# Optimization experiments

Measured on AMD Instinct MI355X. Metric: run time of the kernel, lower is better.

The kernel has to match this reference:

```python
import jax, jax.numpy as jnp
import numpy as np

N_QUBITS = 16
DEPTH = 4
BATCH = 512

# Convention: wire 0 is the most-significant bit of the state index (PennyLane default).

def _rx(t):
    # t: scalar or (B,) real angle -> (2,2) or (B,2,2) complex RX matrix
    h = 0.5 * t
    c = jnp.cos(h).astype(jnp.complex64)
    s = (-1j * jnp.sin(h)).astype(jnp.complex64)
    return jnp.stack([jnp.stack([c, s], -1), jnp.stack([s, c], -1)], -2)

def _ry(t):
    h = 0.5 * t
    c = jnp.cos(h).astype(jnp.complex64)
    s = jnp.sin(h).astype(jnp.complex64)
    return jnp.stack([jnp.stack([c, -s], -1), jnp.stack([s, c], -1)], -2)

def _rz(t):
    e = jnp.exp(-0.5j * t.astype(jnp.complex64))  # diag(e^{-it/2}, e^{+it/2})
    z = jnp.zeros_like(e)
    return jnp.stack([jnp.stack([e, z], -1), jnp.stack([z, jnp.conj(e)], -1)], -2)

def _apply_1q(state, U, q, n):
    # state: (B, 2^n); U: (2,2) shared or (B,2,2) per-batch
    B = state.shape[0]
    L, R = 2 ** q, 2 ** (n - q - 1)
    s = state.reshape(B, L, 2, R)
    if U.ndim == 2:
        s = jnp.einsum('ij,bljr->blir', U, s)
    else:
        s = jnp.einsum('bij,bljr->blir', U, s)
    return s.reshape(B, -1)

def _apply_cnot(state, c, t, n):
    # flips target bit t where control bit c == 1
    B = state.shape[0]
    a, b = min(c, t), max(c, t)
    s = state.reshape(B, 2 ** a, 2, 2 ** (b - a - 1), 2, 2 ** (n - b - 1))
    if c < t:
        # control axis=2, target axis=4
        s1 = s[:, :, 1]                      # (B, 2^a, mid, 2, rest)
        flipped = s1[:, :, :, ::-1, :]
        s = jnp.stack([s[:, :, 0], flipped], axis=2)
    else:
        # control axis=4, target axis=2
        s1 = s[:, :, :, :, 1, :]             # (B, 2^a, 2, mid, rest)
        flipped = s1[:, :, ::-1]
        s = jnp.stack([s[:, :, :, :, 0, :], flipped], axis=4)
    return s.reshape(B, -1)

def _circuit(x, params):
    B, n = x.shape
    depth = params.shape[0]
    state = jnp.zeros((B, 2 ** n), jnp.complex64).at[:, 0].set(1.0)
    # data encoding: batched RX per wire
    for i in range(n):
        state = _apply_1q(state, _rx(x[:, i]), i, n)
    for layer in range(depth):
        for i in range(n):
            # circuit applies RZ then RX then RY -> fuse into one 2x2 matrix
            U = _ry(params[layer, i, 2]) @ _rx(params[layer, i, 1]) @ _rz(params[layer, i, 0])
            state = _apply_1q(state, U, i, n)
        for i in range(n - 1):
            state = _apply_cnot(state, i, i + 1, n)
        state = _apply_cnot(state, n - 1, 0, n)
    # <Z_i> = P(bit_i = 0) - P(bit_i = 1)
    probs = state.real ** 2 + state.imag ** 2
    expz = []
    for i in range(n):
        p = probs.reshape(B, 2 ** i, 2, 2 ** (n - i - 1))
        expz.append(p[:, :, 0].sum((1, 2)) - p[:, :, 1].sum((1, 2)))
    return jnp.stack(expz, axis=1)  # (B, n_qubits)


def setup_inputs() -> dict:
    key = jax.random.key(0)
    k1, k2 = jax.random.split(key)
    x = jax.random.normal(k1, (BATCH, N_QUBITS), dtype=jnp.float32)
    params = jax.random.normal(k2, (DEPTH, N_QUBITS, 3), dtype=jnp.float32)
    return {"x": x, "params": params}


def reference(x, params):
    return _circuit(x, params)
```

## Files before the change

### kernel.cpp

```cpp
#include <hip/hip_runtime.h>


#define NQ 16
#define TPB 256

typedef float __attribute__((ext_vector_type(2))) f2;

__device__ __forceinline__ f2 f2s(float s) { return (f2){s, s}; }

__device__ __forceinline__ f2 cfma(f2 u, f2 a, f2 acc) {
    f2 as = { -a.y, a.x };
    acc = __builtin_elementwise_fma(f2s(u.x), a,  acc);
    acc = __builtin_elementwise_fma(f2s(u.y), as, acc);
    return acc;
}

__device__ __forceinline__ f2 cmulpk(f2 a, f2 b) {
    f2 bs = { -b.y, b.x };
    f2 r = f2s(a.x) * b;
    return __builtin_elementwise_fma(f2s(a.y), bs, r);
}

__device__ __forceinline__ void computeU(const float* params, int layer, int q, f2* U) {
    const float* p = params + (layer*NQ + q)*3;
    float s0, c0, s1, c1, s2, c2;
    sincosf(0.5f*p[0], &s0, &c0);
    sincosf(0.5f*p[1], &s1, &c1);
    sincosf(0.5f*p[2], &s2, &c2);
    f2 m00 = { c1*c0, -c1*s0};
    f2 m01 = { s1*s0, -s1*c0};
    f2 m10 = {-s1*s0, -s1*c0};
    f2 m11 = { c1*c0,  c1*s0};
    U[0] = c2*m00 - s2*m10;
    U[1] = c2*m01 - s2*m11;
    U[2] = s2*m00 + c2*m10;
    U[3] = s2*m01 + c2*m11;
}

template<int MASK>
__device__ __forceinline__ void gate32(f2* A, f2 u00, f2 u01, f2 u10, f2 u11) {
    #pragma unroll
    for (int a = 0; a < 32; ++a) {
        if (!(a & MASK)) {
            f2 x = A[a], y = A[a | MASK];
            f2 xs = { -x.y, x.x };
            f2 ys = { -y.y, y.x };
            f2 nx = f2s(u00.x) * x;
            nx = __builtin_elementwise_fma(f2s(u00.y), xs, nx);
            nx = __builtin_elementwise_fma(f2s(u01.x), y,  nx);
            nx = __builtin_elementwise_fma(f2s(u01.y), ys, nx);
            f2 ny = f2s(u10.x) * x;
            ny = __builtin_elementwise_fma(f2s(u10.y), xs, ny);
            ny = __builtin_elementwise_fma(f2s(u11.x), y,  ny);
            ny = __builtin_elementwise_fma(f2s(u11.y), ys, ny);
            A[a] = nx; A[a | MASK] = ny;
        }
    }
}

__device__ __forceinline__ constexpr int permB(int ad) {
    return (ad & 1)
         | ((((ad >> 1) ^ (ad >> 2)) & 1) << 1)
         | ((((ad >> 2) ^ (ad >> 3)) & 1) << 2)
         | ((((ad >> 3) ^ (ad >> 4)) & 1) << 3)
         | ((((ad >> 4) ^  ad      ) & 1) << 4);
}

__global__ __launch_bounds__(TPB) void qc_gen(
    const float* __restrict__ x, const float* __restrict__ params,
    f2* __restrict__ st)
{
    __shared__ f2 V[16][2];
    const int t    = threadIdx.x;
    const int b    = blockIdx.x >> 3;
    const int fix3 = blockIdx.x & 7;
    f2* base = st + ((size_t)b << NQ) + (fix3 << 13);

    if (t < 16) {
        f2 U[4];
        computeU(params, 0, t, U);
        float s, c;
        sincosf(0.5f * x[b*NQ + t], &s, &c);
        V[15 - t][0] = (f2){U[0].x*c + U[1].y*s, U[0].y*c - U[1].x*s};
        V[15 - t][1] = (f2){U[2].x*c + U[3].y*s, U[2].y*c - U[3].x*s};
    }
    __syncthreads();

    f2 cf = cmulpk(V[0][fix3 & 1], V[1][(fix3 >> 1) & 1]);
    cf = cmulpk(cf, V[2][(fix3 >> 2) & 1]);
    #pragma unroll
    for (int bb = 1; bb <= 7; ++bb)
        cf = cmulpk(cf, V[3 + bb][((t >> (bb - 1)) ^ (t >> bb)) & 1]);

    const int t0 = t & 1, t7 = (t >> 7) & 1;
    float4* dst = (float4*)base;
    #pragma unroll
    for (int h = 0; h < 2; ++h) {
        #pragma unroll
        for (int k = 0; k < 8; ++k) {
            const int k0 = k & 1, k1 = (k >> 1) & 1, k2 = (k >> 2) & 1;
            f2 pk = cmulpk(cf, V[11][t7 ^ k0]);
            pk = cmulpk(pk, V[12][k0 ^ k1]);
            pk = cmulpk(pk, V[13][k1 ^ k2]);
            pk = cmulpk(pk, V[14][k2 ^ h]);
            pk = cmulpk(pk, V[15][h]);
            f2 w0 = cmulpk(pk, V[3][t0]);
            f2 w1 = cmulpk(pk, V[3][1 ^ t0]);
            dst[(t + 256*k) | (h << 11)] = make_float4(w0.x, w0.y, w1.x, w1.y);
        }
    }
}

__global__ __launch_bounds__(TPB, 4) void qc_B_heavy(
    const float* __restrict__ params, f2* __restrict__ st, int lm)
{
    __shared__ __align__(16) f2 S[4096];
    __shared__ f2 Ush[13][4];

    const int t    = threadIdx.x;
    const int b    = blockIdx.x >> 3;
    const int fixb = blockIdx.x & 7;
    f2* base = st + ((size_t)b << NQ);

    if (t < 13) {
        int qb = (t == 0) ? 12 : (t == 1) ? 0 : (t < 5) ? (17 - t) : (16 - t);
        computeU(params, lm, qb, Ush[t]);
    }

    f2 R[32];
    #pragma unroll
    for (int k = 0; k < 16; ++k) {
        int j = 2*(t + 256*k);
        int m = (j & 511) | (fixb << 9) | (((j >> 9) & 1) << 12) | ((j >> 10) << 13);
        float4 v = *(const float4*)(base + m);
        R[2*k]   = (f2){v.x, v.y};
        R[2*k+1] = (f2){v.z, v.w};
    }
    f2 A[32];
    #pragma unroll
    for (int a = 0; a < 32; ++a) A[a] = R[permB(a)];
    __syncthreads();

    gate32<1> (A, Ush[0][0],  Ush[0][1],  Ush[0][2],  Ush[0][3]);
    gate32<2> (A, Ush[1][0],  Ush[1][1],  Ush[1][2],  Ush[1][3]);
    gate32<4> (A, Ush[2][0],  Ush[2][1],  Ush[2][2],  Ush[2][3]);
    gate32<8> (A, Ush[3][0],  Ush[3][1],  Ush[3][2],  Ush[3][3]);
    gate32<16>(A, Ush[4][0],  Ush[4][1],  Ush[4][2],  Ush[4][3]);

    #pragma unroll
    for (int h = 0; h < 2; ++h) {
        __syncthreads();
        #pragma unroll
        for (int c = 0; c < 8; ++c) {
            int slot = ((t << 1) | (c << 9)) ^ (((t >> 4) & 7) << 1);
            f2 a0 = A[h*16 + 2*c], a1 = A[h*16 + 2*c + 1];
            *(float4*)&S[slot] = make_float4(a0.x, a0.y, a1.x, a1.y);
        }
        __syncthreads();
        #pragma unroll
        for (int rr = 0; rr < 16; ++rr) {
            int jj = (t & 1) | (rr << 1) | (((t >> 1) & 15) << 5) | (((t >> 5) & 7) << 9);
            A[h*16 + rr] = S[jj ^ (((t >> 1) & 7) << 1)];
        }
    }

    gate32<1>(A, Ush[5][0], Ush[5][1], Ush[5][2], Ush[5][3]);
    gate32<2>(A, Ush[6][0], Ush[6][1], Ush[6][2], Ush[6][3]);
    gate32<4>(A, Ush[7][0], Ush[7][1], Ush[7][2], Ush[7][3]);
    gate32<8>(A, Ush[8][0], Ush[8][1], Ush[8][2], Ush[8][3]);

    #pragma unroll
    for (int h = 0; h < 2; ++h) {
        __syncthreads();
        #pragma unroll
        for (int rr = 0; rr < 16; ++rr) {
            int jj = (t & 1) | (rr << 1) | (((t >> 1) & 15) << 5) | (((t >> 5) & 7) << 9);
            S[jj ^ (((t >> 1) & 7) << 1)] = A[h*16 + rr];
        }
        __syncthreads();
        #pragma unroll
        for (int rr = 0; rr < 16; ++rr) {
            int jj = (t & 31) | (rr << 5) | (((t >> 5) & 7) << 9);
            A[h*16 + rr] = S[jj ^ ((rr & 7) << 1)];
        }
    }

    gate32<1>(A, Ush[9][0],  Ush[9][1],  Ush[9][2],  Ush[9][3]);
    gate32<2>(A, Ush[10][0], Ush[10][1], Ush[10][2], Ush[10][3]);
    gate32<4>(A, Ush[11][0], Ush[11][1], Ush[11][2], Ush[11][3]);
    gate32<8>(A, Ush[12][0], Ush[12][1], Ush[12][2], Ush[12][3]);

    #pragma unroll
    for (int h = 0; h < 2; ++h) {
        #pragma unroll
        for (int rr = 0; rr < 16; ++rr) {
            int d = (t & 31) | (rr << 5) | (((t >> 5) & 7) << 9) | (h << 12);
            int m = (d & 511) | (fixb << 9) | (((d >> 9) & 1) << 12) | ((d >> 10) << 13);
            base[m] = A[h*16 + rr];
        }
    }
}

__global__ __launch_bounds__(TPB, 4) void qc_A_lite(
    const float* __restrict__ params, f2* __restrict__ st, int layer)
{
    __shared__ __align__(16) f2 S[4096];
    __shared__ f2 Ush[3][4];
    const int t    = threadIdx.x;
    const int b    = blockIdx.x >> 3;
    const int fix3 = blockIdx.x & 7;
    f2* base = st + ((size_t)b << NQ) + (fix3 << 13);

    if (t < 3) computeU(params, layer, 3 - t, Ush[t]);

    f2 A[32];
    const float4* src = (const float4*)base;
    #pragma unroll
    for (int k = 0; k < 16; ++k) {
        float4 v = src[t + 256*k];
        A[2*k]   = (f2){v.x, v.y};
        A[2*k+1] = (f2){v.z, v.w};
    }
    __syncthreads();

    gate32<2>(A, Ush[0][0], Ush[0][1], Ush[0][2], Ush[0][3]);
    gate32<4>(A, Ush[1][0], Ush[1][1], Ush[1][2], Ush[1][3]);
    gate32<8>(A, Ush[2][0], Ush[2][1], Ush[2][2], Ush[2][3]);

    float4* dst = (float4*)base;
    #pragma unroll
    for (int h = 0; h < 2; ++h) {
        __syncthreads();
        #pragma unroll
        for (int c = 0; c < 8; ++c) {
            int slot = ((t << 1) | (c << 9)) ^ (((t >> 4) & 7) << 1);
            f2 a0 = A[h*16 + 2*c], a1 = A[h*16 + 2*c + 1];
            *(float4*)&S[slot] = make_float4(a0.x, a0.y, a1.x, a1.y);
        }
        __syncthreads();
        #pragma unroll
        for (int k = 0; k < 8; ++k) {
            int d  = 2*(t + 256*k);
            int i0 = d ^ (d >> 1) ^ (h << 11);
            int i1 = (d+1) ^ ((d+1) >> 1) ^ (h << 11);
            f2 a0 = S[i0 ^ (((i0 >> 5) & 7) << 1)];
            f2 a1 = S[i1 ^ (((i1 >> 5) & 7) << 1)];
            dst[(t + 256*k) | (h << 11)] = make_float4(a0.x, a0.y, a1.x, a1.y);
        }
    }
}

__global__ __launch_bounds__(TPB) void qc_A_final(
    const float* __restrict__ params, const f2* __restrict__ st,
    float* __restrict__ out)
{
    __shared__ f2 Ush[3][4];
    const int t    = threadIdx.x;
    const int b    = blockIdx.x >> 3;
    const int fix3 = blockIdx.x & 7;
    const f2* base = st + ((size_t)b << NQ) + (fix3 << 13);

    if (t < 3) computeU(params, 3, 3 - t, Ush[t]);

    f2 A[32];
    const float4* src = (const float4*)base;
    #pragma unroll
    for (int k = 0; k < 16; ++k) {
        float4 v = src[t + 256*k];
        A[2*k]   = (f2){v.x, v.y};
        A[2*k+1] = (f2){v.z, v.w};
    }
    __syncthreads();

    gate32<2>(A, Ush[0][0], Ush[0][1], Ush[0][2], Ush[0][3]);
    gate32<4>(A, Ush[1][0], Ush[1][1], Ush[1][2], Ush[1][3]);
    gate32<8>(A, Ush[2][0], Ush[2][1], Ush[2][2], Ush[2][3]);

    float m1 = 0.f, m2 = 0.f, m3 = 0.f, m4 = 0.f, m5 = 0.f;
    #pragma unroll
    for (int a = 0; a < 32; ++a) {
        float p = A[a].x*A[a].x + A[a].y*A[a].y;
        m1 += (__popc(a & 0x1E) & 1) ? -p : p;
        m2 += (__popc(a & 0x1F) & 1) ? -p : p;
        m3 += (__popc(a & 0x1C) & 1) ? -p : p;
        m4 += (__popc(a & 0x18) & 1) ? -p : p;
        m5 += (__popc(a & 0x0F) & 1) ? -p : p;
    }
    const int pt = __popc(t) & 1;
    const int pf = __popc(fix3) & 1;
    float acc[NQ];
    acc[0] = ((pt ^ pf) & 1) ? -m5 : m5;
    acc[1] = m4;
    acc[2] = m3;
    acc[3] = m1;
    #pragma unroll
    for (int q = 4; q <= 11; ++q) {
        int s = __popc(t >> (11 - q)) & 1;
        acc[q] = s ? -m1 : m1;
    }
    acc[12] = pt ? -m2 : m2;
    acc[13] = ((pt ^ (fix3 >> 2)) & 1) ? -m2 : m2;
    acc[14] = ((pt ^ __popc(fix3 >> 1)) & 1) ? -m2 : m2;
    acc[15] = ((pt ^ pf) & 1) ? -m2 : m2;

    #pragma unroll
    for (int q = 0; q < NQ; ++q) {
        float v = acc[q];
        v += __shfl_down(v, 32, 64);
        v += __shfl_down(v, 16, 64);
        v += __shfl_down(v,  8, 64);
        v += __shfl_down(v,  4, 64);
        v += __shfl_down(v,  2, 64);
        v += __shfl_down(v,  1, 64);
        acc[q] = v;
    }
    if ((t & 63) == 0) {
        #pragma unroll
        for (int q = 0; q < NQ; ++q)
            atomicAdd(&out[b*NQ + q], acc[q]);
    }
}

extern "C" void kernel_launch(void* const* d_in, const int* in_sizes, int n_in,
                              void* d_out, int out_size, void* d_ws, size_t ws_size,
                              hipStream_t stream)
{
    (void)in_sizes; (void)n_in; (void)ws_size;
    const float* x      = (const float*)d_in[0];
    const float* params = (const float*)d_in[1];
    float* out = (float*)d_out;
    f2* st = (f2*)d_ws;

    hipMemsetAsync(d_out, 0, (size_t)out_size * sizeof(float), stream);
    qc_gen    <<<dim3(512*8), dim3(TPB), 0, stream>>>(x, params, st);
    qc_B_heavy<<<dim3(512*8), dim3(TPB), 0, stream>>>(params, st, 1);
    qc_A_lite <<<dim3(512*8), dim3(TPB), 0, stream>>>(params, st, 1);
    qc_B_heavy<<<dim3(512*8), dim3(TPB), 0, stream>>>(params, st, 2);
    qc_A_lite <<<dim3(512*8), dim3(TPB), 0, stream>>>(params, st, 2);
    qc_B_heavy<<<dim3(512*8), dim3(TPB), 0, stream>>>(params, st, 3);
    qc_A_final<<<dim3(512*8), dim3(TPB), 0, stream>>>(params, st, out);
}
```

Baseline: 634.9 us.

## Fuse product-state generation into first B-heavy layer kernel

The separate state-generation kernel is removed. The initial product state is now built directly in registers, in the B-kernel's element layout, inside a new fused kernel that then runs the first B-stage gates and stores. This saves one full write and read of the 512x65536 complex state and one launch. In exchange the fused kernel does more per-thread complex multiplies and carries register pressure from the extra temporaries.

```diff
diff --git a/kernel.cpp b/kernel.cpp
--- a/kernel.cpp
+++ b/kernel.cpp
@@ -7,13 +7,6 @@
 typedef float __attribute__((ext_vector_type(2))) f2;
 
 __device__ __forceinline__ f2 f2s(float s) { return (f2){s, s}; }
-
-__device__ __forceinline__ f2 cfma(f2 u, f2 a, f2 acc) {
-    f2 as = { -a.y, a.x };
-    acc = __builtin_elementwise_fma(f2s(u.x), a,  acc);
-    acc = __builtin_elementwise_fma(f2s(u.y), as, acc);
-    return acc;
-}
 
 __device__ __forceinline__ f2 cmulpk(f2 a, f2 b) {
     f2 bs = { -b.y, b.x };
@@ -66,15 +59,81 @@
          | ((((ad >> 4) ^  ad      ) & 1) << 4);
 }
 
-__global__ __launch_bounds__(TPB) void qc_gen(
+__device__ __forceinline__ void b_gates_and_store(
+    f2* A, f2* S, const f2 (*Ush)[4], int t, int fixb, f2* base)
+{
+    gate32<1> (A, Ush[0][0],  Ush[0][1],  Ush[0][2],  Ush[0][3]);
+    gate32<2> (A, Ush[1][0],  Ush[1][1],  Ush[1][2],  Ush[1][3]);
+    gate32<4> (A, Ush[2][0],  Ush[2][1],  Ush[2][2],  Ush[2][3]);
+    gate32<8> (A, Ush[3][0],  Ush[3][1],  Ush[3][2],  Ush[3][3]);
+    gate32<16>(A, Ush[4][0],  Ush[4][1],  Ush[4][2],  Ush[4][3]);
+
+    #pragma unroll
+    for (int h = 0; h < 2; ++h) {
+        __syncthreads();
+        #pragma unroll
+        for (int c = 0; c < 8; ++c) {
+            int slot = ((t << 1) | (c << 9)) ^ (((t >> 4) & 7) << 1);
+            f2 a0 = A[h*16 + 2*c], a1 = A[h*16 + 2*c + 1];
+            *(float4*)&S[slot] = make_float4(a0.x, a0.y, a1.x, a1.y);
+        }
+        __syncthreads();
+        #pragma unroll
+        for (int rr = 0; rr < 16; ++rr) {
+            int jj = (t & 1) | (rr << 1) | (((t >> 1) & 15) << 5) | (((t >> 5) & 7) << 9);
+            A[h*16 + rr] = S[jj ^ (((t >> 1) & 7) << 1)];
+        }
+    }
+
+    gate32<1>(A, Ush[5][0], Ush[5][1], Ush[5][2], Ush[5][3]);
+    gate32<2>(A, Ush[6][0], Ush[6][1], Ush[6][2], Ush[6][3]);
+    gate32<4>(A, Ush[7][0], Ush[7][1], Ush[7][2], Ush[7][3]);
+    gate32<8>(A, Ush[8][0], Ush[8][1], Ush[8][2], Ush[8][3]);
+
+    #pragma unroll
+    for (int h = 0; h < 2; ++h) {
+        __syncthreads();
+        #pragma unroll
+        for (int rr = 0; rr < 16; ++rr) {
+            int jj = (t & 1) | (rr << 1) | (((t >> 1) & 15) << 5) | (((t >> 5) & 7) << 9);
+            S[jj ^ (((t >> 1) & 7) << 1)] = A[h*16 + rr];
+        }
+        __syncthreads();
+        #pragma unroll
+        for (int rr = 0; rr < 16; ++rr) {
+            int jj = (t & 31) | (rr << 5) | (((t >> 5) & 7) << 9);
+            A[h*16 + rr] = S[jj ^ ((rr & 7) << 1)];
+        }
+    }
+
+    gate32<1>(A, Ush[9][0],  Ush[9][1],  Ush[9][2],  Ush[9][3]);
+    gate32<2>(A, Ush[10][0], Ush[10][1], Ush[10][2], Ush[10][3]);
+    gate32<4>(A, Ush[11][0], Ush[11][1], Ush[11][2], Ush[11][3]);
+    gate32<8>(A, Ush[12][0], Ush[12][1], Ush[12][2], Ush[12][3]);
+
+    #pragma unroll
+    for (int h = 0; h < 2; ++h) {
+        #pragma unroll
+        for (int rr = 0; rr < 16; ++rr) {
+            int d = (t & 31) | (rr << 5) | (((t >> 5) & 7) << 9) | (h << 12);
+            int m = (d & 511) | (fixb << 9) | (((d >> 9) & 1) << 12) | ((d >> 10) << 13);
+            base[m] = A[h*16 + rr];
+        }
+    }
+}
+
+__global__ __launch_bounds__(TPB, 4) void qc_B1_gen(
     const float* __restrict__ x, const float* __restrict__ params,
     f2* __restrict__ st)
 {
+    __shared__ __align__(16) f2 S[4096];
+    __shared__ f2 Ush[13][4];
     __shared__ f2 V[16][2];
+
     const int t    = threadIdx.x;
     const int b    = blockIdx.x >> 3;
-    const int fix3 = blockIdx.x & 7;
-    f2* base = st + ((size_t)b << NQ) + (fix3 << 13);
+    const int fixb = blockIdx.x & 7;
+    f2* base = st + ((size_t)b << NQ);
 
     if (t < 16) {
         f2 U[4];
@@ -83,32 +142,53 @@
         sincosf(0.5f * x[b*NQ + t], &s, &c);
         V[15 - t][0] = (f2){U[0].x*c + U[1].y*s, U[0].y*c - U[1].x*s};
         V[15 - t][1] = (f2){U[2].x*c + U[3].y*s, U[2].y*c - U[3].x*s};
+    } else if (t < 29) {
+        int tt = t - 16;
+        int qb = (tt == 0) ? 12 : (tt == 1) ? 0 : (tt < 5) ? (17 - tt) : (16 - tt);
+        computeU(params, 1, qb, Ush[tt]);
     }
     __syncthreads();
 
-    f2 cf = cmulpk(V[0][fix3 & 1], V[1][(fix3 >> 1) & 1]);
-    cf = cmulpk(cf, V[2][(fix3 >> 2) & 1]);
-    #pragma unroll
-    for (int bb = 1; bb <= 7; ++bb)
-        cf = cmulpk(cf, V[3 + bb][((t >> (bb - 1)) ^ (t >> bb)) & 1]);
-
-    const int t0 = t & 1, t7 = (t >> 7) & 1;
-    float4* dst = (float4*)base;
-    #pragma unroll
-    for (int h = 0; h < 2; ++h) {
-        #pragma unroll
-        for (int k = 0; k < 8; ++k) {
-            const int k0 = k & 1, k1 = (k >> 1) & 1, k2 = (k >> 2) & 1;
-            f2 pk = cmulpk(cf, V[11][t7 ^ k0]);
-            pk = cmulpk(pk, V[12][k0 ^ k1]);
-            pk = cmulpk(pk, V[13][k1 ^ k2]);
-            pk = cmulpk(pk, V[14][k2 ^ h]);
-            pk = cmulpk(pk, V[15][h]);
-            f2 w0 = cmulpk(pk, V[3][t0]);
-            f2 w1 = cmulpk(pk, V[3][1 ^ t0]);
-            dst[(t + 256*k) | (h << 11)] = make_float4(w0.x, w0.y, w1.x, w1.y);
-        }
-    }
+    const int f0 = fixb & 1, f1 = (fixb >> 1) & 1, f2b = (fixb >> 2) & 1;
+    const int t0 = t & 1,  t7 = (t >> 7) & 1;
+
+    f2 pre = V[4][(t ^ (t >> 1)) & 1];
+    #pragma unroll
+    for (int bb = 5; bb <= 10; ++bb)
+        pre = cmulpk(pre, V[bb][((t >> (bb - 4)) ^ (t >> (bb - 3))) & 1]);
+    pre = cmulpk(pre, V[11][t7 ^ f0]);
+    pre = cmulpk(pre, V[12][f0 ^ f1]);
+    pre = cmulpk(pre, V[13][f1 ^ f2b]);
+
+    f2 P0 = cmulpk(pre, V[3][t0]);
+    f2 P1 = cmulpk(pre, V[3][1 ^ t0]);
+    f2 Q[4];
+    Q[0] = cmulpk(P0, V[2][0]); Q[1] = cmulpk(P1, V[2][0]);
+    Q[2] = cmulpk(P0, V[2][1]); Q[3] = cmulpk(P1, V[2][1]);
+    f2 Rr[4];
+    Rr[0] = cmulpk(V[0][0], V[1][0]); Rr[1] = cmulpk(V[0][1], V[1][0]);
+    Rr[2] = cmulpk(V[0][0], V[1][1]); Rr[3] = cmulpk(V[0][1], V[1][1]);
+    f2 G0 = cmulpk(V[15][0], V[14][f2b]);
+    f2 G1 = cmulpk(V[15][1], V[14][1 ^ f2b]);
+    f2 TT[8];
+    #pragma unroll
+    for (int e = 0; e < 4; ++e) {
+        TT[2*e]     = cmulpk(G0, Rr[e]);
+        TT[2*e + 1] = cmulpk(G1, Rr[e]);
+    }
+
+    f2 A[32];
+    #pragma unroll
+    for (int a = 0; a < 32; ++a) {
+        const int a0 = a & 1;
+        const int e1 = ((a >> 1) ^ (a >> 2)) & 1;
+        const int e2 = ((a >> 2) ^ (a >> 3)) & 1;
+        const int e3 = ((a >> 3) ^ (a >> 4)) & 1;
+        const int e4 = ((a >> 4) ^  a      ) & 1;
+        A[a] = cmulpk(Q[a0 + 2*e4], TT[e1 + 2*e2 + 4*e3]);
+    }
+
+    b_gates_and_store(A, S, Ush, t, fixb, base);
 }
 
 __global__ __launch_bounds__(TPB, 4) void qc_B_heavy(
@@ -141,64 +221,7 @@
     for (int a = 0; a < 32; ++a) A[a] = R[permB(a)];
     __syncthreads();
 
-    gate32<1> (A, Ush[0][0],  Ush[0][1],  Ush[0][2],  Ush[0][3]);
-    gate32<2> (A, Ush[1][0],  Ush[1][1],  Ush[1][2],  Ush[1][3]);
-    gate32<4> (A, Ush[2][0],  Ush[2][1],  Ush[2][2],  Ush[2][3]);
-    gate32<8> (A, Ush[3][0],  Ush[3][1],  Ush[3][2],  Ush[3][3]);
-    gate32<16>(A, Ush[4][0],  Ush[4][1],  Ush[4][2],  Ush[4][3]);
-
-    #pragma unroll
-    for (int h = 0; h < 2; ++h) {
-        __syncthreads();
-        #pragma unroll
-        for (int c = 0; c < 8; ++c) {
-            int slot = ((t << 1) | (c << 9)) ^ (((t >> 4) & 7) << 1);
-            f2 a0 = A[h*16 + 2*c], a1 = A[h*16 + 2*c + 1];
-            *(float4*)&S[slot] = make_float4(a0.x, a0.y, a1.x, a1.y);
-        }
-        __syncthreads();
-        #pragma unroll
-        for (int rr = 0; rr < 16; ++rr) {
-            int jj = (t & 1) | (rr << 1) | (((t >> 1) & 15) << 5) | (((t >> 5) & 7) << 9);
-            A[h*16 + rr] = S[jj ^ (((t >> 1) & 7) << 1)];
-        }
-    }
-
-    gate32<1>(A, Ush[5][0], Ush[5][1], Ush[5][2], Ush[5][3]);
-    gate32<2>(A, Ush[6][0], Ush[6][1], Ush[6][2], Ush[6][3]);
-    gate32<4>(A, Ush[7][0], Ush[7][1], Ush[7][2], Ush[7][3]);
-    gate32<8>(A, Ush[8][0], Ush[8][1], Ush[8][2], Ush[8][3]);
-
-    #pragma unroll
-    for (int h = 0; h < 2; ++h) {
-        __syncthreads();
-        #pragma unroll
-        for (int rr = 0; rr < 16; ++rr) {
-            int jj = (t & 1) | (rr << 1) | (((t >> 1) & 15) << 5) | (((t >> 5) & 7) << 9);
-            S[jj ^ (((t >> 1) & 7) << 1)] = A[h*16 + rr];
-        }
-        __syncthreads();
-        #pragma unroll
-        for (int rr = 0; rr < 16; ++rr) {
-            int jj = (t & 31) | (rr << 5) | (((t >> 5) & 7) << 9);
-            A[h*16 + rr] = S[jj ^ ((rr & 7) << 1)];
-        }
-    }
-
-    gate32<1>(A, Ush[9][0],  Ush[9][1],  Ush[9][2],  Ush[9][3]);
-    gate32<2>(A, Ush[10][0], Ush[10][1], Ush[10][2], Ush[10][3]);
-    gate32<4>(A, Ush[11][0], Ush[11][1], Ush[11][2], Ush[11][3]);
-    gate32<8>(A, Ush[12][0], Ush[12][1], Ush[12][2], Ush[12][3]);
-
-    #pragma unroll
-    for (int h = 0; h < 2; ++h) {
-        #pragma unroll
-        for (int rr = 0; rr < 16; ++rr) {
-            int d = (t & 31) | (rr << 5) | (((t >> 5) & 7) << 9) | (h << 12);
-            int m = (d & 511) | (fixb << 9) | (((d >> 9) & 1) << 12) | ((d >> 10) << 13);
-            base[m] = A[h*16 + rr];
-        }
-    }
+    b_gates_and_store(A, S, Ush, t, fixb, base);
 }
 
 __global__ __launch_bounds__(TPB, 4) void qc_A_lite(
@@ -332,8 +355,7 @@
     f2* st = (f2*)d_ws;
 
     hipMemsetAsync(d_out, 0, (size_t)out_size * sizeof(float), stream);
-    qc_gen    <<<dim3(512*8), dim3(TPB), 0, stream>>>(x, params, st);
-    qc_B_heavy<<<dim3(512*8), dim3(TPB), 0, stream>>>(params, st, 1);
+    qc_B1_gen <<<dim3(512*8), dim3(TPB), 0, stream>>>(x, params, st);
     qc_A_lite <<<dim3(512*8), dim3(TPB), 0, stream>>>(params, st, 1);
     qc_B_heavy<<<dim3(512*8), dim3(TPB), 0, stream>>>(params, st, 2);
     qc_A_lite <<<dim3(512*8), dim3(TPB), 0, stream>>>(params, st, 2);
```

New measurement: 597.9 us. -5.8%, faster.
